# Kernel tuning notes

Measured on AMD Instinct MI355X. Metric: run time of the kernel, lower is better.

## Reference

```python
import jax, jax.numpy as jnp
import numpy as np

N = 50000      # nodes
E = 800000     # edges (avg degree 16)
D_IN = 128     # in_feats
D_OUT = 128    # out_feats
EPS = 1e-5     # LayerNorm eps


def setup_inputs() -> dict:
    key = jax.random.key(0)
    ks = jax.random.split(key, 8)
    stdv = 1.0 / np.sqrt(5 * D_IN)
    return {
        "h": jax.random.normal(ks[0], (N, D_IN), dtype=jnp.float32),
        "dist": jax.random.uniform(ks[1], (E,), dtype=jnp.float32),
        "W": jax.random.uniform(ks[2], (D_OUT, 5 * D_IN), minval=-stdv, maxval=stdv, dtype=jnp.float32),
        "b": jax.random.uniform(ks[3], (D_OUT,), minval=-stdv, maxval=stdv, dtype=jnp.float32),
        "gamma": jnp.ones((D_OUT,), dtype=jnp.float32),
        "beta": jnp.zeros((D_OUT,), dtype=jnp.float32),
        "src": jax.random.randint(ks[4], (E,), 0, N, dtype=jnp.int32),
        "dst": jax.random.randint(ks[5], (E,), 0, N, dtype=jnp.int32),
        "positions": jax.random.randint(ks[6], (E,), 0, 4, dtype=jnp.int32),
    }


def reference(h, dist, W, b, gamma, beta, src, dst, positions):
    n = h.shape[0]
    h_src = h[src]  # [E, D] gather once, reused by all four directions

    def direction(p):
        # edge-masked u_mul_e + sum aggregation to dst
        w = jnp.where(positions == p, dist, 0.0)
        return jax.ops.segment_sum(h_src * w[:, None], dst, num_segments=n)

    r = direction(0)   # right
    bt = direction(1)  # bottom
    l = direction(2)   # left
    t = direction(0)   # top (original code reuses positions == 0 — faithful)

    cat = jnp.concatenate([h, r, bt, l, t], axis=1)  # [N, 5D]
    z = cat @ W.T + b                                 # [N, D_OUT]
    mu = jnp.mean(z, axis=-1, keepdims=True)
    var = jnp.mean(jnp.square(z - mu), axis=-1, keepdims=True)
    z = (z - mu) * jax.lax.rsqrt(var + EPS) * gamma + beta
    return jax.nn.relu(z)
```

## Files before the change

### kernel.cpp

```cpp
#include <hip/hip_runtime.h>
#include <math.h>
#include <stdint.h>

constexpr int NN = 50000;
constexpr int EE = 800000;
constexpr int D  = 128;
constexpr int CAP = 64;
constexpr int BM = 32;
constexpr int NBX = (NN + BM - 1) / BM;

typedef __attribute__((ext_vector_type(8)))  short bf16x8;
typedef __attribute__((ext_vector_type(16))) float f32x16;

__device__ inline unsigned short f2bf(float x) {
    unsigned u = __builtin_bit_cast(unsigned, x);
    unsigned r = (u + 0x7FFF + ((u >> 16) & 1)) >> 16;
    return (unsigned short)r;
}
__device__ inline float bf2f(unsigned short b) {
    unsigned u = ((unsigned)b) << 16;
    return __builtin_bit_cast(float, u);
}

__global__ __launch_bounds__(256) void prep_wfrag(const float* __restrict__ W,
                                                  unsigned short* __restrict__ Wfh,
                                                  unsigned short* __restrict__ Wfl)
{
    int tid = blockIdx.x * 256 + threadIdx.x;
    int ln  = tid & 31;
    int hs  = (tid >> 5) & 1;
    int s   = (tid >> 6) & 7;
    int vcb = tid >> 9;
    int oc  = vcb * 32 + ln;
    short h8[8], l8[8];
#pragma unroll
    for (int j = 0; j < 8; ++j) {
        int k = s * 16 + hs * 8 + j;
        float v;
        if (oc < 128)      v = W[oc * 640 + k];
        else if (oc < 256) v = W[(oc - 128) * 640 + 128 + k]
                             + W[(oc - 128) * 640 + 512 + k];
        else if (oc < 384) v = W[(oc - 256) * 640 + 256 + k];
        else               v = W[(oc - 384) * 640 + 384 + k];
        unsigned short hb = f2bf(v);
        h8[j] = (short)hb;
        l8[j] = (short)f2bf(v - bf2f(hb));
    }
    *(bf16x8*)(Wfh + (size_t)tid * 8) = *(bf16x8*)h8;
    *(bf16x8*)(Wfl + (size_t)tid * 8) = *(bf16x8*)l8;
}

__global__ __launch_bounds__(256) void fill_bucket(const int* __restrict__ src,
                                                   const int* __restrict__ dst,
                                                   const int* __restrict__ pos,
                                                   const float* __restrict__ dist,
                                                   int* __restrict__ deg,
                                                   int2* __restrict__ bucket)
{
    int e = blockIdx.x * 256 + threadIdx.x;
    if (e >= EE) return;
    int p = pos[e];
    if (p == 3) return;
    int d_ = dst[e];
    int slot = atomicAdd(&deg[d_], 1);
    if (slot < CAP)
        bucket[(size_t)d_ * CAP + slot] =
            make_int2(src[e] * 3 + p, __float_as_int(dist[e]));
}

__global__ __launch_bounds__(256, 8) void pre_gemm(
    const float* __restrict__ h,
    const unsigned short* __restrict__ Wfh, const unsigned short* __restrict__ Wfl,
    const float* __restrict__ bias,
    unsigned short* __restrict__ baseB, unsigned short* __restrict__ Y)
{
    __shared__ __align__(16) short Af[16 * 32 * 8];

    const int t = threadIdx.x;
    const int lane = t & 63;
    const int w = t >> 6;
    const int ln = lane & 31;
    const int hs = lane >> 5;
    const int node0 = blockIdx.x * BM;
    const int by = blockIdx.y;

    {
        int row = t >> 3;
        int g   = t & 7;
        int node = node0 + row;
        float ff[16];
        if (node < NN) {
            const float* hp = h + (size_t)node * D + g * 16;
            float4 f0 = *(const float4*)hp;
            float4 f1 = *(const float4*)(hp + 4);
            float4 f2 = *(const float4*)(hp + 8);
            float4 f3 = *(const float4*)(hp + 12);
            ff[0]=f0.x; ff[1]=f0.y; ff[2]=f0.z; ff[3]=f0.w;
            ff[4]=f1.x; ff[5]=f1.y; ff[6]=f1.z; ff[7]=f1.w;
            ff[8]=f2.x; ff[9]=f2.y; ff[10]=f2.z; ff[11]=f2.w;
            ff[12]=f3.x; ff[13]=f3.y; ff[14]=f3.z; ff[15]=f3.w;
        } else {
#pragma unroll
            for (int j = 0; j < 16; ++j) ff[j] = 0.f;
        }
        short b16[16];
#pragma unroll
        for (int j = 0; j < 16; ++j) b16[j] = (short)f2bf(ff[j]);
        int s0 = 2 * g, s1 = 2 * g + 1;
        *(bf16x8*)(Af + (s0 * 32 + (row ^ s0)) * 8) = *(bf16x8*)&b16[0];
        *(bf16x8*)(Af + (s1 * 32 + (row ^ s1)) * 8) = *(bf16x8*)&b16[8];
    }
    __syncthreads();

    const int vcb = by * 4 + w;

    auto LOADB = [&](int s, bf16x8& bh, bf16x8& bl) {
        size_t fo = ((size_t)((vcb * 8 + s) * 2 + hs) * 32 + ln) * 8;
        bh = *(const bf16x8*)(Wfh + fo);
        bl = *(const bf16x8*)(Wfl + fo);
    };
    auto LOADA = [&](int s) -> bf16x8 {
        int sl = s * 2 + hs;
        return *(const bf16x8*)(Af + (sl * 32 + (ln ^ sl)) * 8);
    };

    f32x16 acc;
#pragma unroll
    for (int i = 0; i < 16; ++i) acc[i] = 0.f;

    bf16x8 bh0, bl0, bh1, bl1;
    LOADB(0, bh0, bl0);
#pragma unroll
    for (int s = 0; s < 8; s += 2) {
        if (s + 1 < 8) LOADB(s + 1, bh1, bl1);
        bf16x8 aa = LOADA(s);
        __builtin_amdgcn_s_setprio(1);
        acc = __builtin_amdgcn_mfma_f32_32x32x16_bf16(aa, bh0, acc, 0, 0, 0);
        acc = __builtin_amdgcn_mfma_f32_32x32x16_bf16(aa, bl0, acc, 0, 0, 0);
        __builtin_amdgcn_s_setprio(0);
        if (s + 2 < 8) LOADB(s + 2, bh0, bl0);
        aa = LOADA(s + 1);
        __builtin_amdgcn_s_setprio(1);
        acc = __builtin_amdgcn_mfma_f32_32x32x16_bf16(aa, bh1, acc, 0, 0, 0);
        acc = __builtin_amdgcn_mfma_f32_32x32x16_bf16(aa, bl1, acc, 0, 0, 0);
        __builtin_amdgcn_s_setprio(0);
    }
    __syncthreads();

    {
        float bc = (by == 0) ? bias[w * 32 + ln] : 0.f;
        unsigned short* Cs = (unsigned short*)Af;
#pragma unroll
        for (int reg = 0; reg < 16; ++reg) {
            int rl = (reg & 3) + 8 * (reg >> 2) + 4 * hs;
            Cs[rl * 128 + w * 32 + ln] = f2bf(acc[reg] + bc);
        }
    }
    __syncthreads();

    {
        const unsigned short* Cs = (const unsigned short*)Af;
        int row = t >> 3;
        int g   = t & 7;
        int grow = node0 + row;
        if (grow < NN) {
            uint2 u0 = *(const uint2*)(Cs + row * 128 + g * 16);
            uint2 u1 = *(const uint2*)(Cs + row * 128 + g * 16 + 4);
            uint2 u2 = *(const uint2*)(Cs + row * 128 + g * 16 + 8);
            uint2 u3 = *(const uint2*)(Cs + row * 128 + g * 16 + 12);
            unsigned short* dp = (by == 0)
                ? baseB + (size_t)grow * D + g * 16
                : Y + ((size_t)grow * 3 + (by - 1)) * D + g * 16;
            *(uint2*)(dp)      = u0;
            *(uint2*)(dp + 4)  = u1;
            *(uint2*)(dp + 8)  = u2;
            *(uint2*)(dp + 12) = u3;
        }
    }
}

__global__ __launch_bounds__(256, 8) void agg_ln(
    const unsigned short* __restrict__ Y, const unsigned short* __restrict__ baseB,
    const int2* __restrict__ bucket, const int* __restrict__ deg,
    const float* __restrict__ gamma, const float* __restrict__ beta,
    float* __restrict__ out)
{
    int w = threadIdx.x >> 6;
    int node = blockIdx.x * 4 + w;
    if (node >= NN) return;
    int lane = threadIdx.x & 63;
    int ln = lane & 31;
    int hs = lane >> 5;

    int n = deg[node];
    if (n > CAP) n = CAP;
    int2 mreg = (lane < n) ? bucket[(size_t)node * CAP + lane] : make_int2(0, 0);

    float a[4] = {0.f, 0.f, 0.f, 0.f};
    for (int b0 = 0; b0 < n; b0 += 16) {
        ushort4 v[8];
        float   wq[8];
#pragma unroll
        for (int j = 0; j < 8; ++j) {
            int idx = b0 + 2 * j + hs;
            int s3 = __shfl(mreg.x, idx, 64);
            int wy = __shfl(mreg.y, idx, 64);
            wq[j] = __int_as_float(wy);
            v[j] = *(const ushort4*)(Y + (size_t)s3 * D + ln * 4);
        }
#pragma unroll
        for (int j = 0; j < 8; ++j) {
            a[0] = fmaf(bf2f(v[j].x), wq[j], a[0]);
            a[1] = fmaf(bf2f(v[j].y), wq[j], a[1]);
            a[2] = fmaf(bf2f(v[j].z), wq[j], a[2]);
            a[3] = fmaf(bf2f(v[j].w), wq[j], a[3]);
        }
    }
#pragma unroll
    for (int c = 0; c < 4; ++c) a[c] += __shfl_xor(a[c], 32, 64);

    ushort4 bv = *(const ushort4*)(baseB + (size_t)node * D + ln * 4);
    float z[4] = {bf2f(bv.x) + a[0], bf2f(bv.y) + a[1],
                  bf2f(bv.z) + a[2], bf2f(bv.w) + a[3]};

    float s = z[0] + z[1] + z[2] + z[3];
    float ss = z[0]*z[0] + z[1]*z[1] + z[2]*z[2] + z[3]*z[3];
#pragma unroll
    for (int m = 1; m < 32; m <<= 1) {
        s  += __shfl_xor(s, m, 64);
        ss += __shfl_xor(ss, m, 64);
    }
    float mu  = s * (1.f / 128.f);
    float var = ss * (1.f / 128.f) - mu * mu;
    float rs  = rsqrtf(var + 1e-5f);

    if (hs == 0) {
        float4 g4 = *(const float4*)(gamma + ln * 4);
        float4 b4 = *(const float4*)(beta + ln * 4);
        float o[4];
        o[0] = (z[0] - mu) * rs * g4.x + b4.x;
        o[1] = (z[1] - mu) * rs * g4.y + b4.y;
        o[2] = (z[2] - mu) * rs * g4.z + b4.z;
        o[3] = (z[3] - mu) * rs * g4.w + b4.w;
#pragma unroll
        for (int c = 0; c < 4; ++c) o[c] = o[c] > 0.f ? o[c] : 0.f;
        *(float4*)(out + (size_t)node * D + ln * 4) = *(float4*)o;
    }
}

extern "C" void kernel_launch(void* const* d_in, const int* in_sizes, int n_in,
                              void* d_out, int out_size, void* d_ws, size_t ws_size,
                              hipStream_t stream)
{
    const float* h     = (const float*)d_in[0];
    const float* dist  = (const float*)d_in[1];
    const float* W     = (const float*)d_in[2];
    const float* bias  = (const float*)d_in[3];
    const float* gamma = (const float*)d_in[4];
    const float* beta  = (const float*)d_in[5];
    const int*   src   = (const int*)d_in[6];
    const int*   dst   = (const int*)d_in[7];
    const int*   pos   = (const int*)d_in[8];

    unsigned short* Wfh   = (unsigned short*)d_ws;
    unsigned short* Wfl   = Wfh + 8192 * 8;
    unsigned short* Y     = Wfl + 8192 * 8;
    unsigned short* baseB = Y + (size_t)NN * 3 * D;
    int*            deg   = (int*)(baseB + (size_t)NN * D);
    int2* bucket = (int2*)(((uintptr_t)(deg + NN) + 15) & ~(uintptr_t)15);

    hipMemsetAsync(deg, 0, NN * sizeof(int), stream);

    prep_wfrag<<<32, 256, 0, stream>>>(W, Wfh, Wfl);
    fill_bucket<<<(EE + 255) / 256, 256, 0, stream>>>(src, dst, pos, dist, deg, bucket);
    pre_gemm<<<dim3(NBX, 4), 256, 0, stream>>>(h, Wfh, Wfl, bias, baseB, Y);
    agg_ln<<<(NN + 3) / 4, 256, 0, stream>>>(Y, baseB, bucket, deg, gamma, beta,
                                             (float*)d_out);
}
```

Before: 185.8 us.

## Fuse bucket fill into GEMM kernel and compute all output columns per block

Zeroing of the degree array moves into the weight-prep kernel, replacing a separate memset. The edge-bucketing kernel and the pre-GEMM are merged into one launch, with extra blocks doing the atomic bucket fill so both can run concurrently. Each GEMM block now computes all 512 output columns for its 32 nodes, so the h tile is loaded and converted once instead of four times. The cost is a 32 KB shared buffer, more accumulator registers, and lower occupancy (launch bounds 2).

Result: faster. 170.8 us (-8.1%).

```diff
diff --git a/kernel.cpp b/kernel.cpp
--- a/kernel.cpp
+++ b/kernel.cpp
@@ -8,6 +8,7 @@
 constexpr int CAP = 64;
 constexpr int BM = 32;
 constexpr int NBX = (NN + BM - 1) / BM;
+constexpr int NBE = (EE + 255) / 256;
 
 typedef __attribute__((ext_vector_type(8)))  short bf16x8;
 typedef __attribute__((ext_vector_type(16))) float f32x16;
@@ -24,7 +25,8 @@
 
 __global__ __launch_bounds__(256) void prep_wfrag(const float* __restrict__ W,
                                                   unsigned short* __restrict__ Wfh,
-                                                  unsigned short* __restrict__ Wfl)
+                                                  unsigned short* __restrict__ Wfl,
+                                                  int* __restrict__ deg)
 {
     int tid = blockIdx.x * 256 + threadIdx.x;
     int ln  = tid & 31;
@@ -48,41 +50,43 @@
     }
     *(bf16x8*)(Wfh + (size_t)tid * 8) = *(bf16x8*)h8;
     *(bf16x8*)(Wfl + (size_t)tid * 8) = *(bf16x8*)l8;
-}
-
-__global__ __launch_bounds__(256) void fill_bucket(const int* __restrict__ src,
-                                                   const int* __restrict__ dst,
-                                                   const int* __restrict__ pos,
-                                                   const float* __restrict__ dist,
-                                                   int* __restrict__ deg,
-                                                   int2* __restrict__ bucket)
-{
-    int e = blockIdx.x * 256 + threadIdx.x;
-    if (e >= EE) return;
-    int p = pos[e];
-    if (p == 3) return;
-    int d_ = dst[e];
-    int slot = atomicAdd(&deg[d_], 1);
-    if (slot < CAP)
-        bucket[(size_t)d_ * CAP + slot] =
-            make_int2(src[e] * 3 + p, __float_as_int(dist[e]));
-}
-
-__global__ __launch_bounds__(256, 8) void pre_gemm(
+
+    for (int i = tid; i < NN; i += 8192) deg[i] = 0;
+}
+
+__global__ __launch_bounds__(256, 2) void fused_mid(
     const float* __restrict__ h,
     const unsigned short* __restrict__ Wfh, const unsigned short* __restrict__ Wfl,
     const float* __restrict__ bias,
-    unsigned short* __restrict__ baseB, unsigned short* __restrict__ Y)
-{
-    __shared__ __align__(16) short Af[16 * 32 * 8];
-
+    unsigned short* __restrict__ baseB, unsigned short* __restrict__ Y,
+    const int* __restrict__ src, const int* __restrict__ dst,
+    const int* __restrict__ pos, const float* __restrict__ dist,
+    int* __restrict__ deg, int2* __restrict__ bucket)
+{
+    __shared__ __align__(16) short CsU[32 * 512];
+
+    if (blockIdx.x >= NBX) {
+        int e = (blockIdx.x - NBX) * 256 + threadIdx.x;
+        if (e < EE) {
+            int p = pos[e];
+            if (p != 3) {
+                int d_ = dst[e];
+                int slot = atomicAdd(&deg[d_], 1);
+                if (slot < CAP)
+                    bucket[(size_t)d_ * CAP + slot] =
+                        make_int2(src[e] * 3 + p, __float_as_int(dist[e]));
+            }
+        }
+        return;
+    }
+
+    short* Af = CsU;
     const int t = threadIdx.x;
     const int lane = t & 63;
     const int w = t >> 6;
     const int ln = lane & 31;
     const int hs = lane >> 5;
     const int node0 = blockIdx.x * BM;
-    const int by = blockIdx.y;
 
     {
         int row = t >> 3;
@@ -112,9 +116,9 @@
     }
     __syncthreads();
 
-    const int vcb = by * 4 + w;
-
-    auto LOADB = [&](int s, bf16x8& bh, bf16x8& bl) {
+    auto LOADB = [&](int st, bf16x8& bh, bf16x8& bl) {
+        int vcb = w * 4 + (st >> 3);
+        int s = st & 7;
         size_t fo = ((size_t)((vcb * 8 + s) * 2 + hs) * 32 + ln) * 8;
         bh = *(const bf16x8*)(Wfh + fo);
         bl = *(const bf16x8*)(Wfl + fo);
@@ -124,57 +128,70 @@
         return *(const bf16x8*)(Af + (sl * 32 + (ln ^ sl)) * 8);
     };
 
-    f32x16 acc;
-#pragma unroll
-    for (int i = 0; i < 16; ++i) acc[i] = 0.f;
+    f32x16 acc[4];
+#pragma unroll
+    for (int q = 0; q < 4; ++q)
+#pragma unroll
+        for (int i = 0; i < 16; ++i) acc[q][i] = 0.f;
 
     bf16x8 bh0, bl0, bh1, bl1;
     LOADB(0, bh0, bl0);
 #pragma unroll
-    for (int s = 0; s < 8; s += 2) {
-        if (s + 1 < 8) LOADB(s + 1, bh1, bl1);
-        bf16x8 aa = LOADA(s);
+    for (int st = 0; st < 32; st += 2) {
+        if (st + 1 < 32) LOADB(st + 1, bh1, bl1);
+        bf16x8 aa = LOADA(st & 7);
         __builtin_amdgcn_s_setprio(1);
-        acc = __builtin_amdgcn_mfma_f32_32x32x16_bf16(aa, bh0, acc, 0, 0, 0);
-        acc = __builtin_amdgcn_mfma_f32_32x32x16_bf16(aa, bl0, acc, 0, 0, 0);
+        acc[st >> 3] = __builtin_amdgcn_mfma_f32_32x32x16_bf16(
+            aa, bh0, acc[st >> 3], 0, 0, 0);
+        acc[st >> 3] = __builtin_amdgcn_mfma_f32_32x32x16_bf16(
+            aa, bl0, acc[st >> 3], 0, 0, 0);
         __builtin_amdgcn_s_setprio(0);
-        if (s + 2 < 8) LOADB(s + 2, bh0, bl0);
-        aa = LOADA(s + 1);
+        if (st + 2 < 32) LOADB(st + 2, bh0, bl0);
+        aa = LOADA((st + 1) & 7);
         __builtin_amdgcn_s_setprio(1);
-        acc = __builtin_amdgcn_mfma_f32_32x32x16_bf16(aa, bh1, acc, 0, 0, 0);
-        acc = __builtin_amdgcn_mfma_f32_32x32x16_bf16(aa, bl1, acc, 0, 0, 0);
+        acc[(st + 1) >> 3] = __builtin_amdgcn_mfma_f32_32x32x16_bf16(
+            aa, bh1, acc[(st + 1) >> 3], 0, 0, 0);
+        acc[(st + 1) >> 3] = __builtin_amdgcn_mfma_f32_32x32x16_bf16(
+            aa, bl1, acc[(st + 1) >> 3], 0, 0, 0);
         __builtin_amdgcn_s_setprio(0);
     }
     __syncthreads();
 
     {
-        float bc = (by == 0) ? bias[w * 32 + ln] : 0.f;
-        unsigned short* Cs = (unsigned short*)Af;
-#pragma unroll
-        for (int reg = 0; reg < 16; ++reg) {
-            int rl = (reg & 3) + 8 * (reg >> 2) + 4 * hs;
-            Cs[rl * 128 + w * 32 + ln] = f2bf(acc[reg] + bc);
+        unsigned short* Cs = (unsigned short*)CsU;
+#pragma unroll
+        for (int q = 0; q < 4; ++q) {
+            int vc = (w * 4 + q) * 32 + ln;
+            float bc = (vc < 128) ? bias[vc] : 0.f;
+#pragma unroll
+            for (int reg = 0; reg < 16; ++reg) {
+                int rl = (reg & 3) + 8 * (reg >> 2) + 4 * hs;
+                Cs[rl * 512 + vc] = f2bf(acc[q][reg] + bc);
+            }
         }
     }
     __syncthreads();
 
     {
-        const unsigned short* Cs = (const unsigned short*)Af;
-        int row = t >> 3;
-        int g   = t & 7;
-        int grow = node0 + row;
-        if (grow < NN) {
-            uint2 u0 = *(const uint2*)(Cs + row * 128 + g * 16);
-            uint2 u1 = *(const uint2*)(Cs + row * 128 + g * 16 + 4);
-            uint2 u2 = *(const uint2*)(Cs + row * 128 + g * 16 + 8);
-            uint2 u3 = *(const uint2*)(Cs + row * 128 + g * 16 + 12);
-            unsigned short* dp = (by == 0)
-                ? baseB + (size_t)grow * D + g * 16
-                : Y + ((size_t)grow * 3 + (by - 1)) * D + g * 16;
-            *(uint2*)(dp)      = u0;
-            *(uint2*)(dp + 4)  = u1;
-            *(uint2*)(dp + 8)  = u2;
-            *(uint2*)(dp + 12) = u3;
+        const unsigned short* Cs = (const unsigned short*)CsU;
+#pragma unroll
+        for (int it = 0; it < 8; ++it) {
+            int c = t + 256 * it;
+            int row = c >> 6;
+            int ci  = c & 63;
+            int vc0 = ci * 8;
+            int node = node0 + row;
+            if (node < NN) {
+                uint2 u0 = *(const uint2*)(Cs + row * 512 + vc0);
+                uint2 u1 = *(const uint2*)(Cs + row * 512 + vc0 + 4);
+                unsigned short* dp;
+                if (vc0 < 128)
+                    dp = baseB + (size_t)node * D + vc0;
+                else
+                    dp = Y + ((size_t)node * 3 + ((vc0 >> 7) - 1)) * D + (vc0 & 127);
+                *(uint2*)dp       = u0;
+                *(uint2*)(dp + 4) = u1;
+            }
         }
     }
 }
@@ -269,11 +286,9 @@
     int*            deg   = (int*)(baseB + (size_t)NN * D);
     int2* bucket = (int2*)(((uintptr_t)(deg + NN) + 15) & ~(uintptr_t)15);
 
-    hipMemsetAsync(deg, 0, NN * sizeof(int), stream);
-
-    prep_wfrag<<<32, 256, 0, stream>>>(W, Wfh, Wfl);
-    fill_bucket<<<(EE + 255) / 256, 256, 0, stream>>>(src, dst, pos, dist, deg, bucket);
-    pre_gemm<<<dim3(NBX, 4), 256, 0, stream>>>(h, Wfh, Wfl, bias, baseB, Y);
+    prep_wfrag<<<32, 256, 0, stream>>>(W, Wfh, Wfl, deg);
+    fused_mid<<<NBX + NBE, 256, 0, stream>>>(h, Wfh, Wfl, bias, baseB, Y,
+                                             src, dst, pos, dist, deg, bucket);
     agg_ln<<<(NN + 3) / 4, 256, 0, stream>>>(Y, baseB, bucket, deg, gamma, beta,
                                              (float*)d_out);
 }
```
